# Kernel optimization log

Measured on AMD Instinct MI355X. Metric: run time of the kernel, lower is better.

The kernel has to match this reference:

```python
import jax, jax.numpy as jnp
import numpy as np

DIM_QK = 64
SCALE = DIM_QK ** 0.5


def setup_inputs() -> dict:
    key = jax.random.key(0)
    kq, kk, kv, kx = jax.random.split(key, 4)
    B, H, N, D = 4, 16, 2048, 64
    Q = jax.random.normal(kq, (B, H, N, D), dtype=jnp.float32)
    K = jax.random.normal(kk, (B, H, N, D), dtype=jnp.float32)
    V = jax.random.normal(kv, (B, H, N, D), dtype=jnp.float32)
    x = jax.random.uniform(kx, (B, 1, N, 1), dtype=jnp.float32)
    return {"Q": Q, "K": K, "V": V, "x": x}


def reference(Q, K, V, x):
    # scores: [B,H,N,N] = Q K^T / sqrt(d_k)  (no softmax)
    scores = jnp.einsum("bhnd,bhmd->bhnm", Q, K) / jnp.asarray(SCALE, Q.dtype)
    # dropout(p=0.0) is identity
    V_scaled = V * x  # broadcast [B,1,N,1] over heads/features
    out = jnp.einsum("bhnm,bhmd->bhnd", scores, V_scaled)
    return out
```

## Files before the change

### kernel.cpp

```cpp
#include <hip/hip_runtime.h>


#define BH 64
#define NROWS 2048
#define DIM 64

__global__ __launch_bounds__(256) void popattn_kv(
    const float* __restrict__ K, const float* __restrict__ V,
    const float* __restrict__ x, float* __restrict__ partial, int nchunk) {
  const int ch = blockIdx.x;
  const int bh = blockIdx.y;
  const int rows = NROWS / nchunk;
  const int m0base = ch * rows;
  const float* Kp = K + (size_t)bh * (NROWS * DIM);
  const float* Vp = V + (size_t)bh * (NROWS * DIM);
  const float* xp = x + (size_t)(bh >> 4) * NROWS;

  __shared__ float smem[4096];
  float (*sK)[DIM] = (float(*)[DIM])smem;
  float (*sV)[DIM] = (float(*)[DIM])(smem + 2048);

  const int t = threadIdx.x;
  const int lr = t >> 4;
  const int lc = (t & 15) << 2;
  const int wv = t >> 6;
  const int l = t & 63;
  const int ti = (l >> 3) << 3;
  const int tj = (l & 7) << 3;

  float acc[8][8];
#pragma unroll
  for (int i = 0; i < 8; ++i)
#pragma unroll
    for (int j = 0; j < 8; ++j) acc[i][j] = 0.f;

  for (int m0 = m0base; m0 < m0base + rows; m0 += 32) {
    const float4 kv0 = *(const float4*)(Kp + (size_t)(m0 + lr) * DIM + lc);
    const float4 kv1 = *(const float4*)(Kp + (size_t)(m0 + 16 + lr) * DIM + lc);
    const float4 vv0 = *(const float4*)(Vp + (size_t)(m0 + lr) * DIM + lc);
    const float4 vv1 = *(const float4*)(Vp + (size_t)(m0 + 16 + lr) * DIM + lc);
    const float xv0 = xp[m0 + lr];
    const float xv1 = xp[m0 + 16 + lr];
    __syncthreads();
    *(float4*)&sK[lr][lc] = kv0;
    *(float4*)&sK[lr + 16][lc] = kv1;
    float4 vs;
    vs.x = vv0.x * xv0; vs.y = vv0.y * xv0; vs.z = vv0.z * xv0; vs.w = vv0.w * xv0;
    *(float4*)&sV[lr][lc] = vs;
    vs.x = vv1.x * xv1; vs.y = vv1.y * xv1; vs.z = vv1.z * xv1; vs.w = vv1.w * xv1;
    *(float4*)&sV[lr + 16][lc] = vs;
    __syncthreads();
#pragma unroll
    for (int mm = 0; mm < 8; ++mm) {
      const int row = wv * 8 + mm;
      const float4 ka0 = *(const float4*)&sK[row][ti];
      const float4 ka1 = *(const float4*)&sK[row][ti + 4];
      const float4 vb0 = *(const float4*)&sV[row][tj];
      const float4 vb1 = *(const float4*)&sV[row][tj + 4];
      const float kk[8] = {ka0.x, ka0.y, ka0.z, ka0.w, ka1.x, ka1.y, ka1.z, ka1.w};
      const float vw[8] = {vb0.x, vb0.y, vb0.z, vb0.w, vb1.x, vb1.y, vb1.z, vb1.w};
#pragma unroll
      for (int ii = 0; ii < 8; ++ii)
#pragma unroll
        for (int jj = 0; jj < 8; ++jj) acc[ii][jj] += kk[ii] * vw[jj];
    }
  }

  __syncthreads();
#pragma unroll 1
  for (int s2 = 0; s2 < 4; ++s2) {
    if (wv == s2) {
#pragma unroll
      for (int ii = 0; ii < 8; ++ii) {
        float* dst = &smem[(ti + ii) * DIM + tj];
        if (s2 == 0) {
          float4 o;
          o.x = acc[ii][0]; o.y = acc[ii][1]; o.z = acc[ii][2]; o.w = acc[ii][3];
          *(float4*)dst = o;
          o.x = acc[ii][4]; o.y = acc[ii][5]; o.z = acc[ii][6]; o.w = acc[ii][7];
          *(float4*)(dst + 4) = o;
        } else {
          float4 a = *(float4*)dst;
          a.x += acc[ii][0]; a.y += acc[ii][1]; a.z += acc[ii][2]; a.w += acc[ii][3];
          *(float4*)dst = a;
          a = *(float4*)(dst + 4);
          a.x += acc[ii][4]; a.y += acc[ii][5]; a.z += acc[ii][6]; a.w += acc[ii][7];
          *(float4*)(dst + 4) = a;
        }
      }
    }
    __syncthreads();
  }

  float* Pp = partial + ((size_t)bh * nchunk + ch) * (DIM * DIM);
#pragma unroll
  for (int i = 0; i < 4; ++i) {
    const int idx = (t + 256 * i) * 4;
    *(float4*)(Pp + idx) = *(const float4*)&smem[idx];
  }
}

__global__ __launch_bounds__(256) void popattn_red(
    const float* __restrict__ partial, float* __restrict__ M, int nchunk) {
  const int e = blockIdx.x;
  const int bh = blockIdx.y;
  const int off = e * 1024 + threadIdx.x * 4;
  const float* Pp = partial + (size_t)bh * nchunk * (DIM * DIM);
  float sx = 0.f, sy = 0.f, sz = 0.f, sw = 0.f;
#pragma unroll 4
  for (int c = 0; c < nchunk; ++c) {
    const float4 p = *(const float4*)(Pp + (size_t)c * (DIM * DIM) + off);
    sx += p.x; sy += p.y; sz += p.z; sw += p.w;
  }
  float4 o;
  o.x = sx * 0.125f; o.y = sy * 0.125f; o.z = sz * 0.125f; o.w = sw * 0.125f;
  *(float4*)(M + (size_t)bh * (DIM * DIM) + off) = o;
}

__global__ __launch_bounds__(256) void popattn_qm(
    const float* __restrict__ Q, const float* __restrict__ M,
    float* __restrict__ out) {
  const int ch = blockIdx.x;
  const int bh = blockIdx.y;
  const int row0 = ch * 256;
  const float* Qp = Q + (size_t)bh * (NROWS * DIM) + (size_t)row0 * DIM;
  float* Op = out + (size_t)bh * (NROWS * DIM) + (size_t)row0 * DIM;

  __shared__ float sM[DIM * DIM];

  const int t = threadIdx.x;
  {
    const float* Mp = M + (size_t)bh * (DIM * DIM);
#pragma unroll
    for (int i = 0; i < 4; ++i) {
      const int off = i * 1024 + t * 4;
      *(float4*)&sM[off] = *(const float4*)(Mp + off);
    }
  }
  __syncthreads();

  const int r = t >> 3;
  const int c8 = (t & 7) * 8;

  float acc[8][8];
#pragma unroll
  for (int rr = 0; rr < 8; ++rr)
#pragma unroll
    for (int jj = 0; jj < 8; ++jj) acc[rr][jj] = 0.f;

#pragma unroll 2
  for (int kg = 0; kg < 16; ++kg) {
    float4 qv[8];
#pragma unroll
    for (int rr = 0; rr < 8; ++rr)
      qv[rr] = *(const float4*)(Qp + (size_t)(r + 32 * rr) * DIM + kg * 4);
#pragma unroll
    for (int dk = 0; dk < 4; ++dk) {
      const int k = kg * 4 + dk;
      const float4 m0 = *(const float4*)&sM[k * DIM + c8];
      const float4 m1 = *(const float4*)&sM[k * DIM + c8 + 4];
      const float mm[8] = {m0.x, m0.y, m0.z, m0.w, m1.x, m1.y, m1.z, m1.w};
#pragma unroll
      for (int rr = 0; rr < 8; ++rr) {
        const float q = (dk == 0) ? qv[rr].x : (dk == 1) ? qv[rr].y
                       : (dk == 2) ? qv[rr].z : qv[rr].w;
#pragma unroll
        for (int jj = 0; jj < 8; ++jj) acc[rr][jj] += q * mm[jj];
      }
    }
  }

#pragma unroll
  for (int rr = 0; rr < 8; ++rr) {
    float4 o;
    o.x = acc[rr][0]; o.y = acc[rr][1]; o.z = acc[rr][2]; o.w = acc[rr][3];
    *(float4*)(Op + (size_t)(r + 32 * rr) * DIM + c8) = o;
    o.x = acc[rr][4]; o.y = acc[rr][5]; o.z = acc[rr][6]; o.w = acc[rr][7];
    *(float4*)(Op + (size_t)(r + 32 * rr) * DIM + c8 + 4) = o;
  }
}

extern "C" void kernel_launch(void* const* d_in, const int* in_sizes, int n_in,
                              void* d_out, int out_size, void* d_ws, size_t ws_size,
                              hipStream_t stream) {
  const float* Q = (const float*)d_in[0];
  const float* K = (const float*)d_in[1];
  const float* V = (const float*)d_in[2];
  const float* x = (const float*)d_in[3];
  float* out = (float*)d_out;
  float* partial = (float*)d_ws;

  int nchunk = 16;
  while (nchunk > 1 &&
         ((size_t)BH * nchunk * DIM * DIM + (size_t)BH * DIM * DIM) * sizeof(float) > ws_size)
    nchunk >>= 1;
  float* Mbuf = partial + (size_t)BH * nchunk * DIM * DIM;

  dim3 blk(256);
  popattn_kv<<<dim3(nchunk, BH), blk, 0, stream>>>(K, V, x, partial, nchunk);
  popattn_red<<<dim3(4, BH), blk, 0, stream>>>(partial, Mbuf, nchunk);
  popattn_qm<<<dim3(NROWS / 256, BH), blk, 0, stream>>>(Q, Mbuf, out);
}
```

Baseline: 53.57 us.

## Fuse partial reduction into QM kernel and load K/V directly from global

Removes the separate reduction kernel: each QM block now sums the 8 per-chunk partial K^T V matrices itself while filling shared memory, saving one launch and one round trip through M. The KV kernel drops the shared-memory staging and block syncs, so each wave reads its own row range of K and V straight from global and multiplies by x in registers. The chunk count is fixed at 8 with launch bounds raised to 2 blocks per SM. In exchange, every QM block redoes the partial reduction (8x redundant partial reads), K/V global loads are less coalesced and duplicated across threads, and the workspace-size fallback is gone.

```diff
diff --git a/kernel.cpp b/kernel.cpp
--- a/kernel.cpp
+++ b/kernel.cpp
@@ -4,25 +4,18 @@
 #define BH 64
 #define NROWS 2048
 #define DIM 64
+#define NCH 8
 
-__global__ __launch_bounds__(256) void popattn_kv(
+__global__ __launch_bounds__(256, 2) void popattn_kv(
     const float* __restrict__ K, const float* __restrict__ V,
-    const float* __restrict__ x, float* __restrict__ partial, int nchunk) {
+    const float* __restrict__ x, float* __restrict__ partial) {
   const int ch = blockIdx.x;
   const int bh = blockIdx.y;
-  const int rows = NROWS / nchunk;
-  const int m0base = ch * rows;
   const float* Kp = K + (size_t)bh * (NROWS * DIM);
   const float* Vp = V + (size_t)bh * (NROWS * DIM);
   const float* xp = x + (size_t)(bh >> 4) * NROWS;
 
-  __shared__ float smem[4096];
-  float (*sK)[DIM] = (float(*)[DIM])smem;
-  float (*sV)[DIM] = (float(*)[DIM])(smem + 2048);
-
   const int t = threadIdx.x;
-  const int lr = t >> 4;
-  const int lc = (t & 15) << 2;
   const int wv = t >> 6;
   const int l = t & 63;
   const int ti = (l >> 3) << 3;
@@ -34,46 +27,32 @@
 #pragma unroll
     for (int j = 0; j < 8; ++j) acc[i][j] = 0.f;
 
-  for (int m0 = m0base; m0 < m0base + rows; m0 += 32) {
-    const float4 kv0 = *(const float4*)(Kp + (size_t)(m0 + lr) * DIM + lc);
-    const float4 kv1 = *(const float4*)(Kp + (size_t)(m0 + 16 + lr) * DIM + lc);
-    const float4 vv0 = *(const float4*)(Vp + (size_t)(m0 + lr) * DIM + lc);
-    const float4 vv1 = *(const float4*)(Vp + (size_t)(m0 + 16 + lr) * DIM + lc);
-    const float xv0 = xp[m0 + lr];
-    const float xv1 = xp[m0 + 16 + lr];
-    __syncthreads();
-    *(float4*)&sK[lr][lc] = kv0;
-    *(float4*)&sK[lr + 16][lc] = kv1;
-    float4 vs;
-    vs.x = vv0.x * xv0; vs.y = vv0.y * xv0; vs.z = vv0.z * xv0; vs.w = vv0.w * xv0;
-    *(float4*)&sV[lr][lc] = vs;
-    vs.x = vv1.x * xv1; vs.y = vv1.y * xv1; vs.z = vv1.z * xv1; vs.w = vv1.w * xv1;
-    *(float4*)&sV[lr + 16][lc] = vs;
-    __syncthreads();
+  const int mstart = ch * (NROWS / NCH) + wv * (NROWS / NCH / 4);
+#pragma unroll 2
+  for (int m = mstart; m < mstart + (NROWS / NCH / 4); ++m) {
+    const float4 k0 = *(const float4*)(Kp + (size_t)m * DIM + ti);
+    const float4 k1 = *(const float4*)(Kp + (size_t)m * DIM + ti + 4);
+    const float4 v0 = *(const float4*)(Vp + (size_t)m * DIM + tj);
+    const float4 v1 = *(const float4*)(Vp + (size_t)m * DIM + tj + 4);
+    const float xv = xp[m];
+    const float kk[8] = {k0.x, k0.y, k0.z, k0.w, k1.x, k1.y, k1.z, k1.w};
+    float vw[8] = {v0.x, v0.y, v0.z, v0.w, v1.x, v1.y, v1.z, v1.w};
 #pragma unroll
-    for (int mm = 0; mm < 8; ++mm) {
-      const int row = wv * 8 + mm;
-      const float4 ka0 = *(const float4*)&sK[row][ti];
-      const float4 ka1 = *(const float4*)&sK[row][ti + 4];
-      const float4 vb0 = *(const float4*)&sV[row][tj];
-      const float4 vb1 = *(const float4*)&sV[row][tj + 4];
-      const float kk[8] = {ka0.x, ka0.y, ka0.z, ka0.w, ka1.x, ka1.y, ka1.z, ka1.w};
-      const float vw[8] = {vb0.x, vb0.y, vb0.z, vb0.w, vb1.x, vb1.y, vb1.z, vb1.w};
+    for (int j = 0; j < 8; ++j) vw[j] *= xv;
 #pragma unroll
-      for (int ii = 0; ii < 8; ++ii)
+    for (int i = 0; i < 8; ++i)
 #pragma unroll
-        for (int jj = 0; jj < 8; ++jj) acc[ii][jj] += kk[ii] * vw[jj];
-    }
+      for (int j = 0; j < 8; ++j) acc[i][j] += kk[i] * vw[j];
   }
 
-  __syncthreads();
+  __shared__ float smem[DIM * DIM];
 #pragma unroll 1
-  for (int s2 = 0; s2 < 4; ++s2) {
-    if (wv == s2) {
+  for (int s = 0; s < 4; ++s) {
+    if (wv == s) {
 #pragma unroll
       for (int ii = 0; ii < 8; ++ii) {
         float* dst = &smem[(ti + ii) * DIM + tj];
-        if (s2 == 0) {
+        if (s == 0) {
           float4 o;
           o.x = acc[ii][0]; o.y = acc[ii][1]; o.z = acc[ii][2]; o.w = acc[ii][3];
           *(float4*)dst = o;
@@ -92,7 +71,7 @@
     __syncthreads();
   }
 
-  float* Pp = partial + ((size_t)bh * nchunk + ch) * (DIM * DIM);
+  float* Pp = partial + ((size_t)bh * NCH + ch) * (DIM * DIM);
 #pragma unroll
   for (int i = 0; i < 4; ++i) {
     const int idx = (t + 256 * i) * 4;
@@ -100,25 +79,8 @@
   }
 }
 
-__global__ __launch_bounds__(256) void popattn_red(
-    const float* __restrict__ partial, float* __restrict__ M, int nchunk) {
-  const int e = blockIdx.x;
-  const int bh = blockIdx.y;
-  const int off = e * 1024 + threadIdx.x * 4;
-  const float* Pp = partial + (size_t)bh * nchunk * (DIM * DIM);
-  float sx = 0.f, sy = 0.f, sz = 0.f, sw = 0.f;
-#pragma unroll 4
-  for (int c = 0; c < nchunk; ++c) {
-    const float4 p = *(const float4*)(Pp + (size_t)c * (DIM * DIM) + off);
-    sx += p.x; sy += p.y; sz += p.z; sw += p.w;
-  }
-  float4 o;
-  o.x = sx * 0.125f; o.y = sy * 0.125f; o.z = sz * 0.125f; o.w = sw * 0.125f;
-  *(float4*)(M + (size_t)bh * (DIM * DIM) + off) = o;
-}
-
-__global__ __launch_bounds__(256) void popattn_qm(
-    const float* __restrict__ Q, const float* __restrict__ M,
+__global__ __launch_bounds__(256, 2) void popattn_qm(
+    const float* __restrict__ Q, const float* __restrict__ partial,
     float* __restrict__ out) {
   const int ch = blockIdx.x;
   const int bh = blockIdx.y;
@@ -130,11 +92,19 @@
 
   const int t = threadIdx.x;
   {
-    const float* Mp = M + (size_t)bh * (DIM * DIM);
+    const float* Pp = partial + (size_t)bh * NCH * (DIM * DIM);
 #pragma unroll
-    for (int i = 0; i < 4; ++i) {
-      const int off = i * 1024 + t * 4;
-      *(float4*)&sM[off] = *(const float4*)(Mp + off);
+    for (int e = 0; e < 4; ++e) {
+      const int off = e * 1024 + t * 4;
+      float sx = 0.f, sy = 0.f, sz = 0.f, sw = 0.f;
+#pragma unroll
+      for (int c = 0; c < NCH; ++c) {
+        const float4 p = *(const float4*)(Pp + (size_t)c * (DIM * DIM) + off);
+        sx += p.x; sy += p.y; sz += p.z; sw += p.w;
+      }
+      float4 o;
+      o.x = sx * 0.125f; o.y = sy * 0.125f; o.z = sz * 0.125f; o.w = sw * 0.125f;
+      *(float4*)&sM[off] = o;
     }
   }
   __syncthreads();
@@ -190,14 +160,7 @@
   float* out = (float*)d_out;
   float* partial = (float*)d_ws;
 
-  int nchunk = 16;
-  while (nchunk > 1 &&
-         ((size_t)BH * nchunk * DIM * DIM + (size_t)BH * DIM * DIM) * sizeof(float) > ws_size)
-    nchunk >>= 1;
-  float* Mbuf = partial + (size_t)BH * nchunk * DIM * DIM;
-
   dim3 blk(256);
-  popattn_kv<<<dim3(nchunk, BH), blk, 0, stream>>>(K, V, x, partial, nchunk);
-  popattn_red<<<dim3(4, BH), blk, 0, stream>>>(partial, Mbuf, nchunk);
-  popattn_qm<<<dim3(NROWS / 256, BH), blk, 0, stream>>>(Q, Mbuf, out);
+  popattn_kv<<<dim3(NCH, BH), blk, 0, stream>>>(K, V, x, partial);
+  popattn_qm<<<dim3(NROWS / 256, BH), blk, 0, stream>>>(Q, partial, out);
 }
```

After: 57.82 us. 1.08x slower.
